# Optimization experiments

Hardware: AMD Instinct MI355X
Metric: run time of the kernel (lower is better)

## Reference

```python
import jax, jax.numpy as jnp
import numpy as np

N_RAYS = 32768
N_SAMPLES = 2097152  # ~64 samples/ray after occupancy-grid culling
HIDDEN = 64
STEP = 0.005  # render_step_size


def setup_inputs() -> dict:
    key = jax.random.key(0)
    ks = jax.random.split(key, 8)
    rays_o = jax.random.normal(ks[0], (N_RAYS, 3), jnp.float32)
    rays_d = jax.random.normal(ks[1], (N_RAYS, 3), jnp.float32)
    rays_d = rays_d / jnp.linalg.norm(rays_d, axis=-1, keepdims=True)
    W1 = jax.random.normal(ks[2], (3, HIDDEN), jnp.float32) * 0.5
    b1 = jnp.zeros((HIDDEN,), jnp.float32)
    W2 = jax.random.normal(ks[3], (HIDDEN, 1), jnp.float32) * 0.1
    b2 = jnp.zeros((1,), jnp.float32)
    # sorted ray indices (occGrid.sampling emits samples grouped by ray)
    ray_indices = jnp.sort(jax.random.randint(ks[4], (N_SAMPLES,), 0, N_RAYS, jnp.int32))
    t_starts = jax.random.uniform(ks[5], (N_SAMPLES,), jnp.float32, 0.2, 2.0)
    t_ends = t_starts + STEP
    return {"rays_o": rays_o, "rays_d": rays_d, "W1": W1, "b1": b1,
            "W2": W2, "b2": b2, "t_starts": t_starts, "t_ends": t_ends,
            "ray_indices": ray_indices, "n_rays": N_RAYS}


def reference(rays_o, rays_d, W1, b1, W2, b2, t_starts, t_ends, ray_indices, n_rays):
    # sigma_fn: gather ray origins/dirs per sample, evaluate density MLP at midpoints
    t_mid = (t_starts + t_ends) * 0.5                       # [S]
    positions = rays_o[ray_indices] + rays_d[ray_indices] * t_mid[:, None]  # [S,3]
    h = jax.nn.relu(positions @ W1 + b1)                    # [S,H]
    sigmas = jax.nn.softplus((h @ W2 + b2)[:, 0])           # [S]

    # render_weight_from_density: per-ray exclusive cumsum of sigma*dt
    s = sigmas * (t_ends - t_starts)                        # [S]
    cum = jnp.cumsum(s)
    excl = cum - s                                          # global exclusive cumsum
    # first sample index of each ray (ray_indices is sorted)
    first_idx = jnp.searchsorted(ray_indices, jnp.arange(n_rays, dtype=ray_indices.dtype))
    offset = excl[first_idx[ray_indices]]                   # exclusive-cumsum at segment start
    trans = jnp.exp(-(excl - offset))                       # per-ray transmittance
    alphas = 1.0 - jnp.exp(-s)
    weights = trans * alphas                                # [S]

    # accumulate_along_rays: segment reductions over rays
    opacities = jax.ops.segment_sum(weights, ray_indices, num_segments=n_rays)
    depth_num = jax.ops.segment_sum(weights * t_mid, ray_indices, num_segments=n_rays)
    depths = depth_num / jnp.clip(opacities, jnp.finfo(opacities.dtype).tiny)
    return jnp.stack([opacities, depths], axis=-1)          # [n_rays, 2]
```

## Files before the change

### kernel.cpp

```cpp
#include <hip/hip_runtime.h>
#include <math.h>

#define HIDDEN 64
#define WAVE_SAMPLES 512
#define SVAL_OFFSET 262144

typedef _Float16 half8   __attribute__((ext_vector_type(8)));
typedef _Float16 half2_t __attribute__((ext_vector_type(2)));
typedef float    f32x16  __attribute__((ext_vector_type(16)));
typedef int      int4_t  __attribute__((ext_vector_type(4)));

template <int CTRL, int RMASK>
__device__ __forceinline__ float dpp_add(float v) {
    int t = __builtin_amdgcn_update_dpp(0, __builtin_bit_cast(int, v),
                                        CTRL, RMASK, 0xF, true);
    return v + __builtin_bit_cast(float, t);
}

__device__ __forceinline__ float bcast_lane(float v, int lane) {
    return __builtin_bit_cast(float,
        __builtin_amdgcn_readlane(__builtin_bit_cast(int, v), lane));
}

__device__ __forceinline__ half2_t pack2(float a, float b) {
    return __builtin_bit_cast(half2_t, __builtin_amdgcn_cvt_pkrtz(a, b));
}

__device__ __forceinline__ half2_t pk_relu(half2_t h) {
    half2_t r;
    asm("v_pk_max_f16 %0, %1, 0" : "=v"(r) : "v"(h));
    return r;
}

__device__ __forceinline__ float scan64(float v) {
    v = dpp_add<0x111, 0xF>(v);
    v = dpp_add<0x112, 0xF>(v);
    v = dpp_add<0x114, 0xF>(v);
    v = dpp_add<0x118, 0xF>(v);
    v = dpp_add<0x142, 0xA>(v);
    v = dpp_add<0x143, 0xC>(v);
    return v;
}

__device__ __forceinline__ float mlp_z(half8 a0, half8 a1,
                                       const half2_t* w2a, const half2_t* w2b,
                                       half8 bf, int xaddr, float bias2) {
    const f32x16 zc = {};
    const f32x16 d0 = __builtin_amdgcn_mfma_f32_32x32x16_f16(a0, bf, zc, 0, 0, 0);
    const f32x16 d1 = __builtin_amdgcn_mfma_f32_32x32x16_f16(a1, bf, zc, 0, 0, 0);
    float c0 = 0.0f, c1 = 0.0f, c2 = 0.0f, c3 = 0.0f;
    #pragma unroll
    for (int r8 = 0; r8 < 8; r8 += 4) {
        c0 = __builtin_amdgcn_fdot2(pk_relu(pack2(d0[2*r8+0], d0[2*r8+1])), w2a[r8+0], c0, false);
        c1 = __builtin_amdgcn_fdot2(pk_relu(pack2(d0[2*r8+2], d0[2*r8+3])), w2a[r8+1], c1, false);
        c2 = __builtin_amdgcn_fdot2(pk_relu(pack2(d0[2*r8+4], d0[2*r8+5])), w2a[r8+2], c2, false);
        c3 = __builtin_amdgcn_fdot2(pk_relu(pack2(d0[2*r8+6], d0[2*r8+7])), w2a[r8+3], c3, false);
    }
    #pragma unroll
    for (int r8 = 0; r8 < 8; r8 += 4) {
        c0 = __builtin_amdgcn_fdot2(pk_relu(pack2(d1[2*r8+0], d1[2*r8+1])), w2b[r8+0], c0, false);
        c1 = __builtin_amdgcn_fdot2(pk_relu(pack2(d1[2*r8+2], d1[2*r8+3])), w2b[r8+1], c1, false);
        c2 = __builtin_amdgcn_fdot2(pk_relu(pack2(d1[2*r8+4], d1[2*r8+5])), w2b[r8+2], c2, false);
        c3 = __builtin_amdgcn_fdot2(pk_relu(pack2(d1[2*r8+6], d1[2*r8+7])), w2b[r8+3], c3, false);
    }
    const float acc = (c0 + c1) + (c2 + c3);
    const int oth = __builtin_amdgcn_ds_bpermute(xaddr, __builtin_bit_cast(int, acc));
    return acc + __builtin_bit_cast(float, oth) + bias2;
}

__global__ __launch_bounds__(256, 4) void mlp_density_kernel(
    const float* __restrict__ rays_o, const float* __restrict__ rays_d,
    const float* __restrict__ W1, const float* __restrict__ b1,
    const float* __restrict__ W2, const float* __restrict__ b2,
    const float* __restrict__ t_starts, const int* __restrict__ ray_indices,
    float* __restrict__ sval_out, int* __restrict__ first_idx,
    int n_samples, int n_rays)
{
    const int tid  = threadIdx.x;
    const int lane = tid & 63;
    const int wave = (blockIdx.x * blockDim.x + tid) >> 6;
    const int n = lane & 31;
    const int q = lane >> 5;

    const int base0 = wave * WAVE_SAMPLES;
    if (base0 >= n_samples) return;
    const int lim = (base0 + WAVE_SAMPLES < n_samples) ? (base0 + WAVE_SAMPLES) : n_samples;

    half8 a0 = {}, a1 = {};
    if (q == 0) {
        const int m = n;
        a0[0] = (_Float16)W1[0 * HIDDEN + m];
        a0[1] = (_Float16)W1[1 * HIDDEN + m];
        a0[2] = (_Float16)W1[2 * HIDDEN + m];
        a0[3] = (_Float16)b1[m];
        a1[0] = (_Float16)W1[0 * HIDDEN + 32 + m];
        a1[1] = (_Float16)W1[1 * HIDDEN + 32 + m];
        a1[2] = (_Float16)W1[2 * HIDDEN + 32 + m];
        a1[3] = (_Float16)b1[32 + m];
    }
    half2_t w2a[8], w2b[8];
    #pragma unroll
    for (int r8 = 0; r8 < 8; ++r8) {
        const int row = 2 * (r8 & 1) + 8 * (r8 >> 1) + 4 * q;
        half2_t pa, pb;
        pa[0] = (_Float16)W2[row];      pa[1] = (_Float16)W2[row + 1];
        pb[0] = (_Float16)W2[row + 32]; pb[1] = (_Float16)W2[row + 33];
        w2a[r8] = pa; w2b[r8] = pb;
    }
    const float bias2 = b2[0];
    const int xaddr = (lane ^ 32) << 2;
    const int bmask = (q == 0) ? ~0 : 0;

    for (int base = base0; base < lim; base += 64) {
        const int iS = base + lane;
        if (iS < n_samples) {
            const int cur  = ray_indices[iS];
            const int prev = (iS == 0) ? -1 : ray_indices[iS - 1];
            for (int r = prev + 1; r <= cur; ++r) first_idx[r] = iS;
            if (iS == n_samples - 1) {
                for (int r = cur + 1; r < n_rays; ++r) first_idx[r] = n_samples;
            }
        }

        const int ia = base + n;
        const int ib = ia + 32;
        const bool va = (ia < n_samples);
        const bool vb = (ib < n_samples);
        const int ca = va ? ia : (n_samples - 1);
        const int cb = vb ? ib : (n_samples - 1);

        const float tsa = t_starts[ca];
        const float tsb = t_starts[cb];
        const int   ria = ray_indices[ca];
        const int   rib = ray_indices[cb];

        const float tm_a = tsa + 0.0025f;
        const float tm_b = tsb + 0.0025f;

        const float oxa = rays_o[3 * ria + 0], oya = rays_o[3 * ria + 1], oza = rays_o[3 * ria + 2];
        const float dxa = rays_d[3 * ria + 0], dya = rays_d[3 * ria + 1], dza = rays_d[3 * ria + 2];
        const float oxb = rays_o[3 * rib + 0], oyb = rays_o[3 * rib + 1], ozb = rays_o[3 * rib + 2];
        const float dxb = rays_d[3 * rib + 0], dyb = rays_d[3 * rib + 1], dzb = rays_d[3 * rib + 2];

        const float pxa = fmaf(dxa, tm_a, oxa);
        const float pya = fmaf(dya, tm_a, oya);
        const float pza = fmaf(dza, tm_a, oza);
        const float pxb = fmaf(dxb, tm_b, oxb);
        const float pyb = fmaf(dyb, tm_b, oyb);
        const float pzb = fmaf(dzb, tm_b, ozb);

        const int a01 = __builtin_bit_cast(int, __builtin_amdgcn_cvt_pkrtz(pxa, pya)) & bmask;
        const int a23 = __builtin_bit_cast(int, __builtin_amdgcn_cvt_pkrtz(pza, 1.0f)) & bmask;
        const int b01 = __builtin_bit_cast(int, __builtin_amdgcn_cvt_pkrtz(pxb, pyb)) & bmask;
        const int b23 = __builtin_bit_cast(int, __builtin_amdgcn_cvt_pkrtz(pzb, 1.0f)) & bmask;
        const int4_t bia = {a01, a23, 0, 0};
        const int4_t bib = {b01, b23, 0, 0};

        const float z_a = mlp_z(a0, a1, w2a, w2b, __builtin_bit_cast(half8, bia), xaddr, bias2);
        const float z_b = mlp_z(a0, a1, w2a, w2b, __builtin_bit_cast(half8, bib), xaddr, bias2);

        const float sg_a = fmaxf(z_a, 0.0f) + __logf(1.0f + __expf(-fabsf(z_a)));
        const float sg_b = fmaxf(z_b, 0.0f) + __logf(1.0f + __expf(-fabsf(z_b)));

        if (q == 0) {
            if (va) sval_out[ia] = sg_a * 0.005f;
            if (vb) sval_out[ib] = sg_b * 0.005f;
        }
    }
}

__global__ __launch_bounds__(256, 8) void render_scan_kernel(
    const float* __restrict__ t_starts, const float* __restrict__ sval,
    const int* __restrict__ first_idx,
    float* __restrict__ out, int n_rays, int n_samples)
{
    const int tid  = threadIdx.x;
    const int lane = tid & 63;
    const int ray  = (blockIdx.x * blockDim.x + tid) >> 6;
    if (ray >= n_rays) return;

    const int seg_start = first_idx[ray];
    const int seg_end   = (ray + 1 < n_rays) ? first_idx[ray + 1] : n_samples;
    if (seg_start >= seg_end) {
        if (lane == 0) { out[2 * ray] = 0.0f; out[2 * ray + 1] = 0.0f; }
        return;
    }

    float carry = 0.0f, op_acc = 0.0f, depth_acc = 0.0f;
    const int last = seg_end - 1;

    for (int base = seg_start; base < seg_end; base += 64) {
        const int  i     = base + lane;
        const bool valid = (i < seg_end);
        const int  ic    = valid ? i : last;

        const float sv = valid ? sval[ic] : 0.0f;
        const float tm = t_starts[ic] + 0.0025f;

        const float scan = scan64(sv);
        const float incl = carry + scan;
        const float w    = __expf(sv - incl) - __expf(-incl);

        op_acc    += w;
        depth_acc  = fmaf(w, tm, depth_acc);
        carry     += bcast_lane(scan, 63);
    }

    const float op_tot = bcast_lane(scan64(op_acc), 63);
    const float dp_tot = bcast_lane(scan64(depth_acc), 63);

    if (lane == 0) {
        const float tiny = 1.17549435e-38f;
        out[2 * ray + 0] = op_tot;
        out[2 * ray + 1] = dp_tot / fmaxf(op_tot, tiny);
    }
}

extern "C" void kernel_launch(void* const* d_in, const int* in_sizes, int n_in,
                              void* d_out, int out_size, void* d_ws, size_t ws_size,
                              hipStream_t stream) {
    const float* rays_o      = (const float*)d_in[0];
    const float* rays_d      = (const float*)d_in[1];
    const float* W1          = (const float*)d_in[2];
    const float* b1          = (const float*)d_in[3];
    const float* W2          = (const float*)d_in[4];
    const float* b2          = (const float*)d_in[5];
    const float* t_starts    = (const float*)d_in[6];
    const int*   ray_indices = (const int*)d_in[8];

    const int n_rays    = in_sizes[0] / 3;
    const int n_samples = in_sizes[6];

    float* out       = (float*)d_out;
    int*   first_idx = (int*)d_ws;
    float* sval      = (float*)((char*)d_ws + SVAL_OFFSET);

    {
        const int waves  = (n_samples + WAVE_SAMPLES - 1) / WAVE_SAMPLES;
        const int blocks = (waves + 3) / 4;
        mlp_density_kernel<<<blocks, 256, 0, stream>>>(
            rays_o, rays_d, W1, b1, W2, b2, t_starts, ray_indices,
            sval, first_idx, n_samples, n_rays);
    }
    {
        const int blocks = (n_rays * 64 + 255) / 256;
        render_scan_kernel<<<blocks, 256, 0, stream>>>(
            t_starts, sval, first_idx, out, n_rays, n_samples);
    }
}
```

Before: 112.5 us.

## Fuse density MLP and per-ray transmittance scan into one ray-blocked kernel

Merges the MLP density kernel and the render scan kernel into a single kernel in which each block owns 32 consecutive rays. The block finds its sample range by binary search over ray_indices, evaluates the MLP for those samples into LDS in chunks of 4096, then each wave scans 8 rays straight from LDS. This removes the global sval and first_idx round trips and the second launch. In exchange it adds a 32 KB LDS buffer that may limit occupancy, per-block binary searches, and extra __syncthreads between the compute and scan phases. Uneven sample counts across blocks can also cause load imbalance.

```diff
diff --git a/kernel.cpp b/kernel.cpp
--- a/kernel.cpp
+++ b/kernel.cpp
@@ -2,8 +2,8 @@
 #include <math.h>
 
 #define HIDDEN 64
-#define WAVE_SAMPLES 512
-#define SVAL_OFFSET 262144
+#define RPB 32
+#define CAP 4096
 
 typedef _Float16 half8   __attribute__((ext_vector_type(8)));
 typedef _Float16 half2_t __attribute__((ext_vector_type(2)));
@@ -68,23 +68,32 @@
     return acc + __builtin_bit_cast(float, oth) + bias2;
 }
 
-__global__ __launch_bounds__(256, 4) void mlp_density_kernel(
+__global__ __launch_bounds__(256, 4) void nerf_fused_kernel(
     const float* __restrict__ rays_o, const float* __restrict__ rays_d,
     const float* __restrict__ W1, const float* __restrict__ b1,
     const float* __restrict__ W2, const float* __restrict__ b2,
     const float* __restrict__ t_starts, const int* __restrict__ ray_indices,
-    float* __restrict__ sval_out, int* __restrict__ first_idx,
-    int n_samples, int n_rays)
+    float* __restrict__ out, int n_rays, int n_samples)
 {
+    __shared__ float2 smp[CAP];
+    __shared__ int    sBounds[RPB + 1];
+
     const int tid  = threadIdx.x;
     const int lane = tid & 63;
-    const int wave = (blockIdx.x * blockDim.x + tid) >> 6;
-    const int n = lane & 31;
-    const int q = lane >> 5;
-
-    const int base0 = wave * WAVE_SAMPLES;
-    if (base0 >= n_samples) return;
-    const int lim = (base0 + WAVE_SAMPLES < n_samples) ? (base0 + WAVE_SAMPLES) : n_samples;
+    const int w    = tid >> 6;
+    const int n    = lane & 31;
+    const int q    = lane >> 5;
+    const int ray0 = blockIdx.x * RPB;
+
+    if (tid <= RPB) {
+        const int target = ray0 + tid;
+        int lo = 0, hi = n_samples;
+        while (lo < hi) {
+            const int mid = (lo + hi) >> 1;
+            if (ray_indices[mid] < target) lo = mid + 1; else hi = mid;
+        }
+        sBounds[tid] = lo;
+    }
 
     half8 a0 = {}, a1 = {};
     if (q == 0) {
@@ -111,108 +120,105 @@
     const int xaddr = (lane ^ 32) << 2;
     const int bmask = (q == 0) ? ~0 : 0;
 
-    for (int base = base0; base < lim; base += 64) {
-        const int iS = base + lane;
-        if (iS < n_samples) {
-            const int cur  = ray_indices[iS];
-            const int prev = (iS == 0) ? -1 : ray_indices[iS - 1];
-            for (int r = prev + 1; r <= cur; ++r) first_idx[r] = iS;
-            if (iS == n_samples - 1) {
-                for (int r = cur + 1; r < n_rays; ++r) first_idx[r] = n_samples;
+    __syncthreads();
+    const int S0 = sBounds[0];
+    const int S1 = sBounds[RPB];
+
+    float carry[8], op[8], dp[8];
+    #pragma unroll
+    for (int k = 0; k < 8; ++k) { carry[k] = 0.0f; op[k] = 0.0f; dp[k] = 0.0f; }
+
+    for (int cs = S0; cs < S1; cs += CAP) {
+        const int ce = (cs + CAP < S1) ? (cs + CAP) : S1;
+
+        for (int base = cs + w * 64; base < ce; base += 256) {
+            const int ia = base + n;
+            const int ib = ia + 32;
+            const bool va = (ia < ce);
+            const bool vb = (ib < ce);
+            const int ca = va ? ia : (ce - 1);
+            const int cb = vb ? ib : (ce - 1);
+
+            const float tm_a = t_starts[ca] + 0.0025f;
+            const float tm_b = t_starts[cb] + 0.0025f;
+            const int   ria  = ray_indices[ca];
+            const int   rib  = ray_indices[cb];
+
+            const float pxa = fmaf(rays_d[3 * ria + 0], tm_a, rays_o[3 * ria + 0]);
+            const float pya = fmaf(rays_d[3 * ria + 1], tm_a, rays_o[3 * ria + 1]);
+            const float pza = fmaf(rays_d[3 * ria + 2], tm_a, rays_o[3 * ria + 2]);
+            const float pxb = fmaf(rays_d[3 * rib + 0], tm_b, rays_o[3 * rib + 0]);
+            const float pyb = fmaf(rays_d[3 * rib + 1], tm_b, rays_o[3 * rib + 1]);
+            const float pzb = fmaf(rays_d[3 * rib + 2], tm_b, rays_o[3 * rib + 2]);
+
+            const int a01 = __builtin_bit_cast(int, __builtin_amdgcn_cvt_pkrtz(pxa, pya)) & bmask;
+            const int a23 = __builtin_bit_cast(int, __builtin_amdgcn_cvt_pkrtz(pza, 1.0f)) & bmask;
+            const int b01 = __builtin_bit_cast(int, __builtin_amdgcn_cvt_pkrtz(pxb, pyb)) & bmask;
+            const int b23 = __builtin_bit_cast(int, __builtin_amdgcn_cvt_pkrtz(pzb, 1.0f)) & bmask;
+            const int4_t bia = {a01, a23, 0, 0};
+            const int4_t bib = {b01, b23, 0, 0};
+
+            const float z_a = mlp_z(a0, a1, w2a, w2b, __builtin_bit_cast(half8, bia), xaddr, bias2);
+            const float z_b = mlp_z(a0, a1, w2a, w2b, __builtin_bit_cast(half8, bib), xaddr, bias2);
+
+            const float sg_a = fmaxf(z_a, 0.0f) + __logf(1.0f + __expf(-fabsf(z_a)));
+            const float sg_b = fmaxf(z_b, 0.0f) + __logf(1.0f + __expf(-fabsf(z_b)));
+
+            if (q == 0) {
+                if (va) smp[ia - cs] = make_float2(sg_a * 0.005f, tm_a);
+                if (vb) smp[ib - cs] = make_float2(sg_b * 0.005f, tm_b);
             }
         }
-
-        const int ia = base + n;
-        const int ib = ia + 32;
-        const bool va = (ia < n_samples);
-        const bool vb = (ib < n_samples);
-        const int ca = va ? ia : (n_samples - 1);
-        const int cb = vb ? ib : (n_samples - 1);
-
-        const float tsa = t_starts[ca];
-        const float tsb = t_starts[cb];
-        const int   ria = ray_indices[ca];
-        const int   rib = ray_indices[cb];
-
-        const float tm_a = tsa + 0.0025f;
-        const float tm_b = tsb + 0.0025f;
-
-        const float oxa = rays_o[3 * ria + 0], oya = rays_o[3 * ria + 1], oza = rays_o[3 * ria + 2];
-        const float dxa = rays_d[3 * ria + 0], dya = rays_d[3 * ria + 1], dza = rays_d[3 * ria + 2];
-        const float oxb = rays_o[3 * rib + 0], oyb = rays_o[3 * rib + 1], ozb = rays_o[3 * rib + 2];
-        const float dxb = rays_d[3 * rib + 0], dyb = rays_d[3 * rib + 1], dzb = rays_d[3 * rib + 2];
-
-        const float pxa = fmaf(dxa, tm_a, oxa);
-        const float pya = fmaf(dya, tm_a, oya);
-        const float pza = fmaf(dza, tm_a, oza);
-        const float pxb = fmaf(dxb, tm_b, oxb);
-        const float pyb = fmaf(dyb, tm_b, oyb);
-        const float pzb = fmaf(dzb, tm_b, ozb);
-
-        const int a01 = __builtin_bit_cast(int, __builtin_amdgcn_cvt_pkrtz(pxa, pya)) & bmask;
-        const int a23 = __builtin_bit_cast(int, __builtin_amdgcn_cvt_pkrtz(pza, 1.0f)) & bmask;
-        const int b01 = __builtin_bit_cast(int, __builtin_amdgcn_cvt_pkrtz(pxb, pyb)) & bmask;
-        const int b23 = __builtin_bit_cast(int, __builtin_amdgcn_cvt_pkrtz(pzb, 1.0f)) & bmask;
-        const int4_t bia = {a01, a23, 0, 0};
-        const int4_t bib = {b01, b23, 0, 0};
-
-        const float z_a = mlp_z(a0, a1, w2a, w2b, __builtin_bit_cast(half8, bia), xaddr, bias2);
-        const float z_b = mlp_z(a0, a1, w2a, w2b, __builtin_bit_cast(half8, bib), xaddr, bias2);
-
-        const float sg_a = fmaxf(z_a, 0.0f) + __logf(1.0f + __expf(-fabsf(z_a)));
-        const float sg_b = fmaxf(z_b, 0.0f) + __logf(1.0f + __expf(-fabsf(z_b)));
-
-        if (q == 0) {
-            if (va) sval_out[ia] = sg_a * 0.005f;
-            if (vb) sval_out[ib] = sg_b * 0.005f;
-        }
-    }
-}
-
-__global__ __launch_bounds__(256, 8) void render_scan_kernel(
-    const float* __restrict__ t_starts, const float* __restrict__ sval,
-    const int* __restrict__ first_idx,
-    float* __restrict__ out, int n_rays, int n_samples)
-{
-    const int tid  = threadIdx.x;
-    const int lane = tid & 63;
-    const int ray  = (blockIdx.x * blockDim.x + tid) >> 6;
-    if (ray >= n_rays) return;
-
-    const int seg_start = first_idx[ray];
-    const int seg_end   = (ray + 1 < n_rays) ? first_idx[ray + 1] : n_samples;
-    if (seg_start >= seg_end) {
-        if (lane == 0) { out[2 * ray] = 0.0f; out[2 * ray + 1] = 0.0f; }
-        return;
-    }
-
-    float carry = 0.0f, op_acc = 0.0f, depth_acc = 0.0f;
-    const int last = seg_end - 1;
-
-    for (int base = seg_start; base < seg_end; base += 64) {
-        const int  i     = base + lane;
-        const bool valid = (i < seg_end);
-        const int  ic    = valid ? i : last;
-
-        const float sv = valid ? sval[ic] : 0.0f;
-        const float tm = t_starts[ic] + 0.0025f;
-
-        const float scan = scan64(sv);
-        const float incl = carry + scan;
-        const float w    = __expf(sv - incl) - __expf(-incl);
-
-        op_acc    += w;
-        depth_acc  = fmaf(w, tm, depth_acc);
-        carry     += bcast_lane(scan, 63);
-    }
-
-    const float op_tot = bcast_lane(scan64(op_acc), 63);
-    const float dp_tot = bcast_lane(scan64(depth_acc), 63);
-
-    if (lane == 0) {
-        const float tiny = 1.17549435e-38f;
-        out[2 * ray + 0] = op_tot;
-        out[2 * ray + 1] = dp_tot / fmaxf(op_tot, tiny);
+        __syncthreads();
+
+        #pragma unroll
+        for (int k = 0; k < 8; ++k) {
+            const int r = w * 8 + k;
+            const int seg_start = sBounds[r];
+            const int seg_end   = sBounds[r + 1];
+            const int lo = (seg_start > cs) ? seg_start : cs;
+            const int hi = (seg_end   < ce) ? seg_end   : ce;
+
+            float c = carry[k], o = op[k], d = dp[k];
+            for (int base = lo; base < hi; base += 64) {
+                const int  i     = base + lane;
+                const bool valid = (i < hi);
+                const int  idx   = (valid ? i : (hi - 1)) - cs;
+
+                const float2 v  = smp[idx];
+                const float  sv = valid ? v.x : 0.0f;
+
+                const float scn  = scan64(sv);
+                const float incl = c + scn;
+                const float wt   = __expf(sv - incl) - __expf(-incl);
+
+                o += wt;
+                d  = fmaf(wt, v.y, d);
+                c += bcast_lane(scn, 63);
+            }
+            carry[k] = c; op[k] = o; dp[k] = d;
+        }
+        __syncthreads();
+    }
+
+    #pragma unroll
+    for (int k = 0; k < 8; ++k) {
+        const int r = ray0 + w * 8 + k;
+        if (r >= n_rays) continue;
+        const float op_tot = bcast_lane(scan64(op[k]), 63);
+        const float dp_tot = bcast_lane(scan64(dp[k]), 63);
+        if (lane == 0) {
+            const int seg_start = sBounds[w * 8 + k];
+            const int seg_end   = sBounds[w * 8 + k + 1];
+            if (seg_start >= seg_end) {
+                out[2 * r + 0] = 0.0f;
+                out[2 * r + 1] = 0.0f;
+            } else {
+                const float tiny = 1.17549435e-38f;
+                out[2 * r + 0] = op_tot;
+                out[2 * r + 1] = dp_tot / fmaxf(op_tot, tiny);
+            }
+        }
     }
 }
 
@@ -231,20 +237,10 @@
     const int n_rays    = in_sizes[0] / 3;
     const int n_samples = in_sizes[6];
 
-    float* out       = (float*)d_out;
-    int*   first_idx = (int*)d_ws;
-    float* sval      = (float*)((char*)d_ws + SVAL_OFFSET);
-
-    {
-        const int waves  = (n_samples + WAVE_SAMPLES - 1) / WAVE_SAMPLES;
-        const int blocks = (waves + 3) / 4;
-        mlp_density_kernel<<<blocks, 256, 0, stream>>>(
-            rays_o, rays_d, W1, b1, W2, b2, t_starts, ray_indices,
-            sval, first_idx, n_samples, n_rays);
-    }
-    {
-        const int blocks = (n_rays * 64 + 255) / 256;
-        render_scan_kernel<<<blocks, 256, 0, stream>>>(
-            t_starts, sval, first_idx, out, n_rays, n_samples);
-    }
-}
+    float* out = (float*)d_out;
+
+    const int blocks = (n_rays + RPB - 1) / RPB;
+    nerf_fused_kernel<<<blocks, 256, 0, stream>>>(
+        rays_o, rays_d, W1, b1, W2, b2, t_starts, ray_indices,
+        out, n_rays, n_samples);
+}
```

Measured after the change: 115.6 us. +2.8%, slower.
